# Kernel tuning notes

Hardware: AMD Instinct MI355X
Metric: run time of the kernel (lower is better)

Reference implementation:

```python
import jax, jax.numpy as jnp
import numpy as np


def _avg_conv(x, k):
    # depthwise k x k box filter, same padding (torch F.conv2d groups=C)
    C = x.shape[1]
    w = jnp.ones((C, 1, k, k), x.dtype) / (k * k)
    return jax.lax.conv_general_dilated(
        x, w, window_strides=(1, 1),
        padding=[(k // 2, k // 2), (k // 2, k // 2)],
        feature_group_count=C,
        dimension_numbers=('NCHW', 'OIHW', 'NCHW'))


def _shift_feat(where, features, neig_avg_size):
    # Faithful port of shiftFeat: edge-replicate shift + 1e-4 mask on padded strip,
    # then depthwise box average when neig_avg_size > 1. dilation is overridden to
    # neig_avg_size // 2 when neig_avg_size > 1 (as in the torch code).
    B, C, H, W = features.shape
    d = neig_avg_size // 2 if neig_avg_size > 1 else 1
    dt = features.dtype
    PAD = jnp.asarray(1e-4, dt)
    if where == 'none':
        fs = features
        m = jnp.ones((B, 1, H, W), dt)
    elif where == 'left':
        pad = jnp.broadcast_to(features[:, :, :, -1:], (B, C, H, d))
        fs = jnp.concatenate([features[:, :, :, d:], pad], axis=3)
        m = jnp.concatenate([jnp.ones((B, 1, H, W - d), dt), jnp.full((B, 1, H, d), PAD, dt)], axis=3)
    elif where == 'right':
        pad = jnp.broadcast_to(features[:, :, :, :1], (B, C, H, d))
        fs = jnp.concatenate([pad, features[:, :, :, :-d]], axis=3)
        m = jnp.concatenate([jnp.full((B, 1, H, d), PAD, dt), jnp.ones((B, 1, H, W - d), dt)], axis=3)
    elif where == 'bot':
        pad = jnp.broadcast_to(features[:, :, :1, :], (B, C, d, W))
        fs = jnp.concatenate([pad, features[:, :, :-d, :]], axis=2)
        m = jnp.concatenate([jnp.full((B, 1, d, W), PAD, dt), jnp.ones((B, 1, H - d, W), dt)], axis=2)
    elif where == 'top':
        pad = jnp.broadcast_to(features[:, :, -1:, :], (B, C, d, W))
        fs = jnp.concatenate([features[:, :, d:, :], pad], axis=2)
        m = jnp.concatenate([jnp.ones((B, 1, H - d, W), dt), jnp.full((B, 1, d, W), PAD, dt)], axis=2)
    else:
        raise ValueError('Unknown position')
    if neig_avg_size > 1:
        fs = _avg_conv(fs, neig_avg_size)
    # torch takes mask.mean(dim=1, keepdim=True); mask is constant across channels
    return fs, m


def _cos_sim(f1, m1, f2, m2):
    num = (f1 * f2 * m1 * m2).sum(axis=1, keepdims=True)
    den = (jnp.sqrt(((m1 * f1) ** 2).sum(axis=1, keepdims=True))
           * jnp.sqrt(((m2 * f2) ** 2).sum(axis=1, keepdims=True)))
    return num / den


def _total_sim(features, k):
    f1, m1 = _shift_feat('right', features, k)
    f2, m2 = _shift_feat('left', features, k)
    horiz = _cos_sim(f1, m1, f2, m2)
    f1, m1 = _shift_feat('top', features, k)
    f2, m2 = _shift_feat('bot', features, k)
    verti = _cos_sim(f1, m1, f2, m2)
    return (horiz + verti) / 2  # [B,1,H,W]


def setup_inputs() -> dict:
    key = jax.random.key(0)
    features = jax.random.normal(key, (16, 512, 56, 56), dtype=jnp.float32)
    return {"features": features, "patch_sim_neiref_neisimavgsize": 3}


def reference(features, patch_sim_neiref_neisimavgsize):
    return _total_sim(features, patch_sim_neiref_neisimavgsize)
```

## Files before the change

### kernel.cpp

```cpp
#include <hip/hip_runtime.h>
#include <hip/hip_bf16.h>

#define BB 16
#define CC 512
#define HH 56
#define WW 56
#define HW (HH * WW)
#define NPIX (BB * HW)
#define CGROUPS 8

typedef float v4f __attribute__((ext_vector_type(4)));

__device__ __forceinline__ float shfl64(float v, int srcLane) {
    return __shfl(v, srcLane, 64);
}

template <int NITER, bool WRITE_OUT>
__global__ __launch_bounds__(256, 4) void ComputeTotalSim_84267258347855_kernel(
    const float* __restrict__ feat, float* __restrict__ ws, float* __restrict__ out) {
    const int wave = threadIdx.x >> 6;
    const int lane = threadIdx.x & 63;
    const int sc = lane >> 4;
    const int q = lane & 15;
    const int qs = (q <= 13) ? q : 13;
    const int x0 = 4 * qs;
    const int b = blockIdx.z;
    const int cg = blockIdx.x;
    const int y = blockIdx.y * 4 + wave;

    const float mym = (y >= 1) ? 1.f : 0.f;
    const float myp = (y <= HH - 2) ? 1.f : 0.f;
    const float mxm0 = (q == 0) ? 0.f : 1.f;
    const float mxp3 = (q >= 13) ? 0.f : 1.f;

    const int ry0 = (y - 2 < 0) ? 0 : y - 2;
    const int ry1 = (y - 1 < 0) ? 0 : y - 1;
    const int ry3 = (y + 1 > HH - 1) ? HH - 1 : y + 1;
    const int ry4 = (y + 2 > HH - 1) ? HH - 1 : y + 2;
    const int o0 = ry0 * WW + x0, o1 = ry1 * WW + x0, o2 = y * WW + x0,
              o3 = ry3 * WW + x0, o4 = ry4 * WW + x0;

    const float* p = feat + ((size_t)b * CC + (size_t)cg * (4 * NITER) + sc) * HW;

    float sA0 = 0, sA1 = 0, sA2 = 0, sA3 = 0;
    float sB0 = 0, sB1 = 0, sB2 = 0, sB3 = 0;
    float sC0 = 0, sC1 = 0, sC2 = 0, sC3 = 0;
    float sD0 = 0, sD1 = 0, sD2 = 0, sD3 = 0;
    float sE0 = 0, sE1 = 0, sE2 = 0, sE3 = 0;
    float sF0 = 0, sF1 = 0, sF2 = 0, sF3 = 0;

#define STEP(A0, A1, A2, A3, A4)                                                \
    {                                                                           \
        const float Vx = fmaf(mym, A1.x, fmaf(myp, A3.x, A2.x));                \
        const float Vy = fmaf(mym, A1.y, fmaf(myp, A3.y, A2.y));                \
        const float Vz = fmaf(mym, A1.z, fmaf(myp, A3.z, A2.z));                \
        const float Vw = fmaf(mym, A1.w, fmaf(myp, A3.w, A2.w));                \
        const float t3x = fmaf(mym, A2.x, fmaf(myp, A4.x, A3.x));               \
        const float t3y = fmaf(mym, A2.y, fmaf(myp, A4.y, A3.y));               \
        const float t3z = fmaf(mym, A2.z, fmaf(myp, A4.z, A3.z));               \
        const float t3w = fmaf(mym, A2.w, fmaf(myp, A4.w, A3.w));               \
        const float t4x = fmaf(mym, A0.x, fmaf(myp, A2.x, A1.x));               \
        const float t4y = fmaf(mym, A0.y, fmaf(myp, A2.y, A1.y));               \
        const float t4z = fmaf(mym, A0.z, fmaf(myp, A2.z, A1.z));               \
        const float t4w = fmaf(mym, A0.w, fmaf(myp, A2.w, A1.w));               \
        float Vm2 = shfl64(Vz, lane - 1), Vm1 = shfl64(Vw, lane - 1);           \
        float Vp4 = shfl64(Vx, lane + 1), Vp5 = shfl64(Vy, lane + 1);           \
        float w3m = shfl64(t3w, lane - 1), w3p = shfl64(t3x, lane + 1);         \
        float w4m = shfl64(t4w, lane - 1), w4p = shfl64(t4x, lane + 1);         \
        if (q == 0) { Vm2 = Vx; Vm1 = Vx; w3m = t3x; w4m = t4x; }               \
        if (q >= 13) { Vp4 = Vw; Vp5 = Vw; w3p = t3w; w4p = t4w; }              \
        const float f10 = fmaf(mxm0, Vm2, Vm1 + Vx);                            \
        const float f11 = Vm1 + Vx + Vy;                                        \
        const float f12 = Vx + Vy + Vz;                                         \
        const float f13 = fmaf(mxp3, Vw, Vy + Vz);                              \
        const float f20 = fmaf(mxm0, Vx, Vy + Vz);                              \
        const float f21 = Vy + Vz + Vw;                                         \
        const float f22 = Vz + Vw + Vp4;                                        \
        const float f23 = fmaf(mxp3, Vp5, Vw + Vp4);                            \
        const float f30 = fmaf(mxm0, w3m, t3x + t3y);                           \
        const float f31 = t3x + t3y + t3z;                                      \
        const float f32 = t3y + t3z + t3w;                                      \
        const float f33 = fmaf(mxp3, w3p, t3z + t3w);                           \
        const float f40 = fmaf(mxm0, w4m, t4x + t4y);                           \
        const float f41 = t4x + t4y + t4z;                                      \
        const float f42 = t4y + t4z + t4w;                                      \
        const float f43 = fmaf(mxp3, w4p, t4z + t4w);                           \
        sA0 = fmaf(f10, f20, sA0); sA1 = fmaf(f11, f21, sA1);                   \
        sA2 = fmaf(f12, f22, sA2); sA3 = fmaf(f13, f23, sA3);                   \
        sB0 = fmaf(f10, f10, sB0); sB1 = fmaf(f11, f11, sB1);                   \
        sB2 = fmaf(f12, f12, sB2); sB3 = fmaf(f13, f13, sB3);                   \
        sC0 = fmaf(f20, f20, sC0); sC1 = fmaf(f21, f21, sC1);                   \
        sC2 = fmaf(f22, f22, sC2); sC3 = fmaf(f23, f23, sC3);                   \
        sD0 = fmaf(f30, f40, sD0); sD1 = fmaf(f31, f41, sD1);                   \
        sD2 = fmaf(f32, f42, sD2); sD3 = fmaf(f33, f43, sD3);                   \
        sE0 = fmaf(f30, f30, sE0); sE1 = fmaf(f31, f31, sE1);                   \
        sE2 = fmaf(f32, f32, sE2); sE3 = fmaf(f33, f33, sE3);                   \
        sF0 = fmaf(f40, f40, sF0); sF1 = fmaf(f41, f41, sF1);                   \
        sF2 = fmaf(f42, f42, sF2); sF3 = fmaf(f43, f43, sF3);                   \
    }

#define LOAD5(R0, R1, R2, R3, R4, PC)                                                      \
    asm volatile("global_load_dwordx4 %0, %1, off offset:-448" : "=&v"(R0) : "v"(PC));     \
    asm volatile("global_load_dwordx4 %0, %1, off offset:-224" : "=&v"(R1) : "v"(PC));     \
    asm volatile("global_load_dwordx4 %0, %1, off"             : "=&v"(R2) : "v"(PC));     \
    asm volatile("global_load_dwordx4 %0, %1, off offset:224"  : "=&v"(R3) : "v"(PC));     \
    asm volatile("global_load_dwordx4 %0, %1, off offset:448"  : "=&v"(R4) : "v"(PC));

#define WAITV(N)                                          \
    asm volatile("s_waitcnt vmcnt(" #N ")" ::: "memory"); \
    __builtin_amdgcn_sched_barrier(0);

    v4f A0, A1, A2, A3, A4, B0, B1, B2, B3, B4;

    if (blockIdx.y >= 1 && blockIdx.y <= 12) {
        const float* pc = p + o2;
        LOAD5(A0, A1, A2, A3, A4, pc); pc += 4 * HW;
        LOAD5(B0, B1, B2, B3, B4, pc); pc += 4 * HW;
        for (int k = 0; k + 4 <= NITER; k += 2) {
            WAITV(5);
            STEP(A0, A1, A2, A3, A4);
            LOAD5(A0, A1, A2, A3, A4, pc); pc += 4 * HW;
            WAITV(5);
            STEP(B0, B1, B2, B3, B4);
            LOAD5(B0, B1, B2, B3, B4, pc); pc += 4 * HW;
        }
        WAITV(5);
        STEP(A0, A1, A2, A3, A4);
        WAITV(0);
        STEP(B0, B1, B2, B3, B4);
    } else {
        A0 = *(const v4f*)(p + o0); A1 = *(const v4f*)(p + o1);
        A2 = *(const v4f*)(p + o2); A3 = *(const v4f*)(p + o3);
        A4 = *(const v4f*)(p + o4);
        p += 4 * HW;
        for (int k = 0; k + 2 <= NITER; k += 2) {
            B0 = *(const v4f*)(p + o0); B1 = *(const v4f*)(p + o1);
            B2 = *(const v4f*)(p + o2); B3 = *(const v4f*)(p + o3);
            B4 = *(const v4f*)(p + o4);
            STEP(A0, A1, A2, A3, A4);
            const float* pn = (k + 2 < NITER) ? p + 4 * HW : p;
            A0 = *(const v4f*)(pn + o0); A1 = *(const v4f*)(pn + o1);
            A2 = *(const v4f*)(pn + o2); A3 = *(const v4f*)(pn + o3);
            A4 = *(const v4f*)(pn + o4);
            STEP(B0, B1, B2, B3, B4);
            p = pn + 4 * HW;
        }
    }
#undef STEP
#undef LOAD5
#undef WAITV

#define RED2(v) { v += __shfl_xor(v, 16, 64); v += __shfl_xor(v, 32, 64); }
    RED2(sA0) RED2(sA1) RED2(sA2) RED2(sA3)
    RED2(sB0) RED2(sB1) RED2(sB2) RED2(sB3)
    RED2(sC0) RED2(sC1) RED2(sC2) RED2(sC3)
    RED2(sD0) RED2(sD1) RED2(sD2) RED2(sD3)
    RED2(sE0) RED2(sE1) RED2(sE2) RED2(sE3)
    RED2(sF0) RED2(sF1) RED2(sF2) RED2(sF3)
#undef RED2

    if (lane < 14) {
        const int pix = b * HW + y * WW + 4 * q;
        if (WRITE_OUT) {
            v4f r;
            r.x = (float)(0.5 * ((double)sA0 / sqrt((double)sB0 * (double)sC0) +
                                 (double)sD0 / sqrt((double)sE0 * (double)sF0)));
            r.y = (float)(0.5 * ((double)sA1 / sqrt((double)sB1 * (double)sC1) +
                                 (double)sD1 / sqrt((double)sE1 * (double)sF1)));
            r.z = (float)(0.5 * ((double)sA2 / sqrt((double)sB2 * (double)sC2) +
                                 (double)sD2 / sqrt((double)sE2 * (double)sF2)));
            r.w = (float)(0.5 * ((double)sA3 / sqrt((double)sB3 * (double)sC3) +
                                 (double)sD3 / sqrt((double)sE3 * (double)sF3)));
            *(v4f*)(out + pix) = r;
        } else {
            float* slab = ws + (size_t)cg * 6 * NPIX;
            *(v4f*)(slab + 0 * NPIX + pix) = (v4f){sA0, sA1, sA2, sA3};
            *(v4f*)(slab + 1 * NPIX + pix) = (v4f){sB0, sB1, sB2, sB3};
            *(v4f*)(slab + 2 * NPIX + pix) = (v4f){sC0, sC1, sC2, sC3};
            *(v4f*)(slab + 3 * NPIX + pix) = (v4f){sD0, sD1, sD2, sD3};
            *(v4f*)(slab + 4 * NPIX + pix) = (v4f){sE0, sE1, sE2, sE3};
            *(v4f*)(slab + 5 * NPIX + pix) = (v4f){sF0, sF1, sF2, sF3};
        }
    }
}

__global__ void ComputeTotalSim_finalize(const float* __restrict__ ws,
                                         float* __restrict__ out) {
    const int i = blockIdx.x * blockDim.x + threadIdx.x;
    if (i < NPIX) {
        double a0 = 0, a1 = 0, a2 = 0, a3 = 0, a4 = 0, a5 = 0;
#pragma unroll
        for (int cg = 0; cg < CGROUPS; ++cg) {
            const float* slab = ws + (size_t)cg * 6 * NPIX;
            a0 += slab[0 * NPIX + i];
            a1 += slab[1 * NPIX + i];
            a2 += slab[2 * NPIX + i];
            a3 += slab[3 * NPIX + i];
            a4 += slab[4 * NPIX + i];
            a5 += slab[5 * NPIX + i];
        }
        out[i] = (float)(0.5 * (a0 / sqrt(a1 * a2) + a3 / sqrt(a4 * a5)));
    }
}

extern "C" void kernel_launch(void* const* d_in, const int* in_sizes, int n_in,
                              void* d_out, int out_size, void* d_ws, size_t ws_size,
                              hipStream_t stream) {
    const float* feat = (const float*)d_in[0];
    float* out = (float*)d_out;

    const size_t need = (size_t)CGROUPS * 6 * NPIX * sizeof(float);
    if (ws_size >= need) {
        dim3 grid(CGROUPS, HH / 4, BB);
        ComputeTotalSim_84267258347855_kernel<CC / (4 * CGROUPS), false>
            <<<grid, 256, 0, stream>>>(feat, (float*)d_ws, out);
        ComputeTotalSim_finalize<<<(NPIX + 255) / 256, 256, 0, stream>>>(
            (const float*)d_ws, out);
    } else {
        dim3 grid(1, HH / 4, BB);
        ComputeTotalSim_84267258347855_kernel<CC / 4, true>
            <<<grid, 256, 0, stream>>>(feat, nullptr, out);
    }
}
```

Before: 34.10 us.

## Compute two output rows per wave with shared vertical sums and doubled channel groups

Each wave now produces two adjacent output rows. It loads six input rows instead of five per row and shares the vertical 3-row sums between the two rows' shifted box filters. This cuts global loads per output row from five to three and reuses intermediate sums. Channel groups go from 8 to 16 to keep the grid size up while blocks handle 8 rows. The cost is double the accumulator registers and a larger workspace and finalize reduction, which may lower occupancy.

```diff
diff --git a/kernel.cpp b/kernel.cpp
--- a/kernel.cpp
+++ b/kernel.cpp
@@ -7,7 +7,7 @@
 #define WW 56
 #define HW (HH * WW)
 #define NPIX (BB * HW)
-#define CGROUPS 8
+#define CGROUPS 16
 
 typedef float v4f __attribute__((ext_vector_type(4)));
 
@@ -20,147 +20,196 @@
     const float* __restrict__ feat, float* __restrict__ ws, float* __restrict__ out) {
     const int wave = threadIdx.x >> 6;
     const int lane = threadIdx.x & 63;
+    const int q = lane & 15;
     const int sc = lane >> 4;
-    const int q = lane & 15;
     const int qs = (q <= 13) ? q : 13;
     const int x0 = 4 * qs;
     const int b = blockIdx.z;
     const int cg = blockIdx.x;
-    const int y = blockIdx.y * 4 + wave;
-
-    const float mym = (y >= 1) ? 1.f : 0.f;
-    const float myp = (y <= HH - 2) ? 1.f : 0.f;
+    const int ys = blockIdx.y * 8 + 2 * wave;
+
     const float mxm0 = (q == 0) ? 0.f : 1.f;
     const float mxp3 = (q >= 13) ? 0.f : 1.f;
 
-    const int ry0 = (y - 2 < 0) ? 0 : y - 2;
-    const int ry1 = (y - 1 < 0) ? 0 : y - 1;
-    const int ry3 = (y + 1 > HH - 1) ? HH - 1 : y + 1;
-    const int ry4 = (y + 2 > HH - 1) ? HH - 1 : y + 2;
-    const int o0 = ry0 * WW + x0, o1 = ry1 * WW + x0, o2 = y * WW + x0,
-              o3 = ry3 * WW + x0, o4 = ry4 * WW + x0;
-
     const float* p = feat + ((size_t)b * CC + (size_t)cg * (4 * NITER) + sc) * HW;
 
-    float sA0 = 0, sA1 = 0, sA2 = 0, sA3 = 0;
-    float sB0 = 0, sB1 = 0, sB2 = 0, sB3 = 0;
-    float sC0 = 0, sC1 = 0, sC2 = 0, sC3 = 0;
-    float sD0 = 0, sD1 = 0, sD2 = 0, sD3 = 0;
-    float sE0 = 0, sE1 = 0, sE2 = 0, sE3 = 0;
-    float sF0 = 0, sF1 = 0, sF2 = 0, sF3 = 0;
-
-#define STEP(A0, A1, A2, A3, A4)                                                \
-    {                                                                           \
-        const float Vx = fmaf(mym, A1.x, fmaf(myp, A3.x, A2.x));                \
-        const float Vy = fmaf(mym, A1.y, fmaf(myp, A3.y, A2.y));                \
-        const float Vz = fmaf(mym, A1.z, fmaf(myp, A3.z, A2.z));                \
-        const float Vw = fmaf(mym, A1.w, fmaf(myp, A3.w, A2.w));                \
-        const float t3x = fmaf(mym, A2.x, fmaf(myp, A4.x, A3.x));               \
-        const float t3y = fmaf(mym, A2.y, fmaf(myp, A4.y, A3.y));               \
-        const float t3z = fmaf(mym, A2.z, fmaf(myp, A4.z, A3.z));               \
-        const float t3w = fmaf(mym, A2.w, fmaf(myp, A4.w, A3.w));               \
-        const float t4x = fmaf(mym, A0.x, fmaf(myp, A2.x, A1.x));               \
-        const float t4y = fmaf(mym, A0.y, fmaf(myp, A2.y, A1.y));               \
-        const float t4z = fmaf(mym, A0.z, fmaf(myp, A2.z, A1.z));               \
-        const float t4w = fmaf(mym, A0.w, fmaf(myp, A2.w, A1.w));               \
-        float Vm2 = shfl64(Vz, lane - 1), Vm1 = shfl64(Vw, lane - 1);           \
-        float Vp4 = shfl64(Vx, lane + 1), Vp5 = shfl64(Vy, lane + 1);           \
-        float w3m = shfl64(t3w, lane - 1), w3p = shfl64(t3x, lane + 1);         \
-        float w4m = shfl64(t4w, lane - 1), w4p = shfl64(t4x, lane + 1);         \
-        if (q == 0) { Vm2 = Vx; Vm1 = Vx; w3m = t3x; w4m = t4x; }               \
-        if (q >= 13) { Vp4 = Vw; Vp5 = Vw; w3p = t3w; w4p = t4w; }              \
-        const float f10 = fmaf(mxm0, Vm2, Vm1 + Vx);                            \
-        const float f11 = Vm1 + Vx + Vy;                                        \
-        const float f12 = Vx + Vy + Vz;                                         \
-        const float f13 = fmaf(mxp3, Vw, Vy + Vz);                              \
-        const float f20 = fmaf(mxm0, Vx, Vy + Vz);                              \
-        const float f21 = Vy + Vz + Vw;                                         \
-        const float f22 = Vz + Vw + Vp4;                                        \
-        const float f23 = fmaf(mxp3, Vp5, Vw + Vp4);                            \
-        const float f30 = fmaf(mxm0, w3m, t3x + t3y);                           \
-        const float f31 = t3x + t3y + t3z;                                      \
-        const float f32 = t3y + t3z + t3w;                                      \
-        const float f33 = fmaf(mxp3, w3p, t3z + t3w);                           \
-        const float f40 = fmaf(mxm0, w4m, t4x + t4y);                           \
-        const float f41 = t4x + t4y + t4z;                                      \
-        const float f42 = t4y + t4z + t4w;                                      \
-        const float f43 = fmaf(mxp3, w4p, t4z + t4w);                           \
-        sA0 = fmaf(f10, f20, sA0); sA1 = fmaf(f11, f21, sA1);                   \
-        sA2 = fmaf(f12, f22, sA2); sA3 = fmaf(f13, f23, sA3);                   \
-        sB0 = fmaf(f10, f10, sB0); sB1 = fmaf(f11, f11, sB1);                   \
-        sB2 = fmaf(f12, f12, sB2); sB3 = fmaf(f13, f13, sB3);                   \
-        sC0 = fmaf(f20, f20, sC0); sC1 = fmaf(f21, f21, sC1);                   \
-        sC2 = fmaf(f22, f22, sC2); sC3 = fmaf(f23, f23, sC3);                   \
-        sD0 = fmaf(f30, f40, sD0); sD1 = fmaf(f31, f41, sD1);                   \
-        sD2 = fmaf(f32, f42, sD2); sD3 = fmaf(f33, f43, sD3);                   \
-        sE0 = fmaf(f30, f30, sE0); sE1 = fmaf(f31, f31, sE1);                   \
-        sE2 = fmaf(f32, f32, sE2); sE3 = fmaf(f33, f33, sE3);                   \
-        sF0 = fmaf(f40, f40, sF0); sF1 = fmaf(f41, f41, sF1);                   \
-        sF2 = fmaf(f42, f42, sF2); sF3 = fmaf(f43, f43, sF3);                   \
-    }
-
-#define LOAD5(R0, R1, R2, R3, R4, PC)                                                      \
+    float sA0 = 0, sA1 = 0, sA2 = 0, sA3 = 0, sB0 = 0, sB1 = 0, sB2 = 0, sB3 = 0;
+    float sC0 = 0, sC1 = 0, sC2 = 0, sC3 = 0, sD0 = 0, sD1 = 0, sD2 = 0, sD3 = 0;
+    float sE0 = 0, sE1 = 0, sE2 = 0, sE3 = 0, sF0 = 0, sF1 = 0, sF2 = 0, sF3 = 0;
+    float tA0 = 0, tA1 = 0, tA2 = 0, tA3 = 0, tB0 = 0, tB1 = 0, tB2 = 0, tB3 = 0;
+    float tC0 = 0, tC1 = 0, tC2 = 0, tC3 = 0, tD0 = 0, tD1 = 0, tD2 = 0, tD3 = 0;
+    float tE0 = 0, tE1 = 0, tE2 = 0, tE3 = 0, tF0 = 0, tF1 = 0, tF2 = 0, tF3 = 0;
+
+#define SHARED2(R0, R1, R2, R3, R4, R5)                                          \
+    {                                                                            \
+        const v4f t12 = R1 + R2, t34 = R3 + R4;                                  \
+        const v4f Sa = R0 + t12, Sb = t12 + R3, Sc = t34 + R2, Sd = t34 + R5;    \
+        float aL = shfl64(Sa.w, lane - 1), aR = shfl64(Sa.x, lane + 1);          \
+        float bL2 = shfl64(Sb.z, lane - 1), bL1 = shfl64(Sb.w, lane - 1);        \
+        float bR1 = shfl64(Sb.x, lane + 1), bR2 = shfl64(Sb.y, lane + 1);        \
+        float cL2 = shfl64(Sc.z, lane - 1), cL1 = shfl64(Sc.w, lane - 1);        \
+        float cR1 = shfl64(Sc.x, lane + 1), cR2 = shfl64(Sc.y, lane + 1);        \
+        float dL = shfl64(Sd.w, lane - 1), dR = shfl64(Sd.x, lane + 1);          \
+        if (q == 0) { aL = Sa.x; bL2 = Sb.x; bL1 = Sb.x; cL2 = Sc.x; cL1 = Sc.x; dL = Sd.x; } \
+        if (q >= 13) { aR = Sa.w; bR1 = Sb.w; bR2 = Sb.w; cR1 = Sc.w; cR2 = Sc.w; dR = Sd.w; } \
+        {                                        \
+            const float f10 = fmaf(mxm0, bL2, bL1 + Sb.x), f11 = bL1 + Sb.x + Sb.y;  \
+            const float f12 = Sb.x + Sb.y + Sb.z, f13 = fmaf(mxp3, Sb.w, Sb.y + Sb.z); \
+            const float f20 = fmaf(mxm0, Sb.x, Sb.y + Sb.z), f21 = Sb.y + Sb.z + Sb.w; \
+            const float f22 = Sb.z + Sb.w + bR1, f23 = fmaf(mxp3, bR2, Sb.w + bR1);  \
+            const float f30 = fmaf(mxm0, cL1, Sc.x + Sc.y), f31 = Sc.x + Sc.y + Sc.z; \
+            const float f32 = Sc.y + Sc.z + Sc.w, f33 = fmaf(mxp3, cR1, Sc.z + Sc.w); \
+            const float f40 = fmaf(mxm0, aL, Sa.x + Sa.y), f41 = Sa.x + Sa.y + Sa.z; \
+            const float f42 = Sa.y + Sa.z + Sa.w, f43 = fmaf(mxp3, aR, Sa.z + Sa.w); \
+            sA0 = fmaf(f10, f20, sA0); sA1 = fmaf(f11, f21, sA1);                \
+            sA2 = fmaf(f12, f22, sA2); sA3 = fmaf(f13, f23, sA3);                \
+            sB0 = fmaf(f10, f10, sB0); sB1 = fmaf(f11, f11, sB1);                \
+            sB2 = fmaf(f12, f12, sB2); sB3 = fmaf(f13, f13, sB3);                \
+            sC0 = fmaf(f20, f20, sC0); sC1 = fmaf(f21, f21, sC1);                \
+            sC2 = fmaf(f22, f22, sC2); sC3 = fmaf(f23, f23, sC3);                \
+            sD0 = fmaf(f30, f40, sD0); sD1 = fmaf(f31, f41, sD1);                \
+            sD2 = fmaf(f32, f42, sD2); sD3 = fmaf(f33, f43, sD3);                \
+            sE0 = fmaf(f30, f30, sE0); sE1 = fmaf(f31, f31, sE1);                \
+            sE2 = fmaf(f32, f32, sE2); sE3 = fmaf(f33, f33, sE3);                \
+            sF0 = fmaf(f40, f40, sF0); sF1 = fmaf(f41, f41, sF1);                \
+            sF2 = fmaf(f42, f42, sF2); sF3 = fmaf(f43, f43, sF3);                \
+        }                                                                        \
+        {                                      \
+            const float f10 = fmaf(mxm0, cL2, cL1 + Sc.x), f11 = cL1 + Sc.x + Sc.y;  \
+            const float f12 = Sc.x + Sc.y + Sc.z, f13 = fmaf(mxp3, Sc.w, Sc.y + Sc.z); \
+            const float f20 = fmaf(mxm0, Sc.x, Sc.y + Sc.z), f21 = Sc.y + Sc.z + Sc.w; \
+            const float f22 = Sc.z + Sc.w + cR1, f23 = fmaf(mxp3, cR2, Sc.w + cR1);  \
+            const float f30 = fmaf(mxm0, dL, Sd.x + Sd.y), f31 = Sd.x + Sd.y + Sd.z; \
+            const float f32 = Sd.y + Sd.z + Sd.w, f33 = fmaf(mxp3, dR, Sd.z + Sd.w); \
+            const float f40 = fmaf(mxm0, bL1, Sb.x + Sb.y), f41 = Sb.x + Sb.y + Sb.z; \
+            const float f42 = Sb.y + Sb.z + Sb.w, f43 = fmaf(mxp3, bR1, Sb.z + Sb.w); \
+            tA0 = fmaf(f10, f20, tA0); tA1 = fmaf(f11, f21, tA1);                \
+            tA2 = fmaf(f12, f22, tA2); tA3 = fmaf(f13, f23, tA3);                \
+            tB0 = fmaf(f10, f10, tB0); tB1 = fmaf(f11, f11, tB1);                \
+            tB2 = fmaf(f12, f12, tB2); tB3 = fmaf(f13, f13, tB3);                \
+            tC0 = fmaf(f20, f20, tC0); tC1 = fmaf(f21, f21, tC1);                \
+            tC2 = fmaf(f22, f22, tC2); tC3 = fmaf(f23, f23, tC3);                \
+            tD0 = fmaf(f30, f40, tD0); tD1 = fmaf(f31, f41, tD1);                \
+            tD2 = fmaf(f32, f42, tD2); tD3 = fmaf(f33, f43, tD3);                \
+            tE0 = fmaf(f30, f30, tE0); tE1 = fmaf(f31, f31, tE1);                \
+            tE2 = fmaf(f32, f32, tE2); tE3 = fmaf(f33, f33, tE3);                \
+            tF0 = fmaf(f40, f40, tF0); tF1 = fmaf(f41, f41, tF1);                \
+            tF2 = fmaf(f42, f42, tF2); tF3 = fmaf(f43, f43, tF3);                \
+        }                                                                        \
+    }
+
+#define STEPB(A0_, A1_, A2_, A3_, A4_, MYM, MYP, P)                              \
+    {                                                                            \
+        const float Vx = fmaf(MYM, A1_.x, fmaf(MYP, A3_.x, A2_.x));              \
+        const float Vy = fmaf(MYM, A1_.y, fmaf(MYP, A3_.y, A2_.y));              \
+        const float Vz = fmaf(MYM, A1_.z, fmaf(MYP, A3_.z, A2_.z));              \
+        const float Vw = fmaf(MYM, A1_.w, fmaf(MYP, A3_.w, A2_.w));              \
+        const float u3x = fmaf(MYM, A2_.x, fmaf(MYP, A4_.x, A3_.x));             \
+        const float u3y = fmaf(MYM, A2_.y, fmaf(MYP, A4_.y, A3_.y));             \
+        const float u3z = fmaf(MYM, A2_.z, fmaf(MYP, A4_.z, A3_.z));             \
+        const float u3w = fmaf(MYM, A2_.w, fmaf(MYP, A4_.w, A3_.w));             \
+        const float u4x = fmaf(MYM, A0_.x, fmaf(MYP, A2_.x, A1_.x));             \
+        const float u4y = fmaf(MYM, A0_.y, fmaf(MYP, A2_.y, A1_.y));             \
+        const float u4z = fmaf(MYM, A0_.z, fmaf(MYP, A2_.z, A1_.z));             \
+        const float u4w = fmaf(MYM, A0_.w, fmaf(MYP, A2_.w, A1_.w));             \
+        float Vm2 = shfl64(Vz, lane - 1), Vm1 = shfl64(Vw, lane - 1);            \
+        float Vp4 = shfl64(Vx, lane + 1), Vp5 = shfl64(Vy, lane + 1);            \
+        float w3m = shfl64(u3w, lane - 1), w3p = shfl64(u3x, lane + 1);          \
+        float w4m = shfl64(u4w, lane - 1), w4p = shfl64(u4x, lane + 1);          \
+        if (q == 0) { Vm2 = Vx; Vm1 = Vx; w3m = u3x; w4m = u4x; }                \
+        if (q >= 13) { Vp4 = Vw; Vp5 = Vw; w3p = u3w; w4p = u4w; }               \
+        const float f10 = fmaf(mxm0, Vm2, Vm1 + Vx), f11 = Vm1 + Vx + Vy;        \
+        const float f12 = Vx + Vy + Vz, f13 = fmaf(mxp3, Vw, Vy + Vz);           \
+        const float f20 = fmaf(mxm0, Vx, Vy + Vz), f21 = Vy + Vz + Vw;           \
+        const float f22 = Vz + Vw + Vp4, f23 = fmaf(mxp3, Vp5, Vw + Vp4);        \
+        const float f30 = fmaf(mxm0, w3m, u3x + u3y), f31 = u3x + u3y + u3z;     \
+        const float f32 = u3y + u3z + u3w, f33 = fmaf(mxp3, w3p, u3z + u3w);     \
+        const float f40 = fmaf(mxm0, w4m, u4x + u4y), f41 = u4x + u4y + u4z;     \
+        const float f42 = u4y + u4z + u4w, f43 = fmaf(mxp3, w4p, u4z + u4w);     \
+        P##A0 = fmaf(f10, f20, P##A0); P##A1 = fmaf(f11, f21, P##A1);            \
+        P##A2 = fmaf(f12, f22, P##A2); P##A3 = fmaf(f13, f23, P##A3);            \
+        P##B0 = fmaf(f10, f10, P##B0); P##B1 = fmaf(f11, f11, P##B1);            \
+        P##B2 = fmaf(f12, f12, P##B2); P##B3 = fmaf(f13, f13, P##B3);            \
+        P##C0 = fmaf(f20, f20, P##C0); P##C1 = fmaf(f21, f21, P##C1);            \
+        P##C2 = fmaf(f22, f22, P##C2); P##C3 = fmaf(f23, f23, P##C3);            \
+        P##D0 = fmaf(f30, f40, P##D0); P##D1 = fmaf(f31, f41, P##D1);            \
+        P##D2 = fmaf(f32, f42, P##D2); P##D3 = fmaf(f33, f43, P##D3);            \
+        P##E0 = fmaf(f30, f30, P##E0); P##E1 = fmaf(f31, f31, P##E1);            \
+        P##E2 = fmaf(f32, f32, P##E2); P##E3 = fmaf(f33, f33, P##E3);            \
+        P##F0 = fmaf(f40, f40, P##F0); P##F1 = fmaf(f41, f41, P##F1);            \
+        P##F2 = fmaf(f42, f42, P##F2); P##F3 = fmaf(f43, f43, P##F3);            \
+    }
+
+#define LOAD6(R0, R1, R2, R3, R4, R5, PC)                                                  \
     asm volatile("global_load_dwordx4 %0, %1, off offset:-448" : "=&v"(R0) : "v"(PC));     \
     asm volatile("global_load_dwordx4 %0, %1, off offset:-224" : "=&v"(R1) : "v"(PC));     \
     asm volatile("global_load_dwordx4 %0, %1, off"             : "=&v"(R2) : "v"(PC));     \
     asm volatile("global_load_dwordx4 %0, %1, off offset:224"  : "=&v"(R3) : "v"(PC));     \
-    asm volatile("global_load_dwordx4 %0, %1, off offset:448"  : "=&v"(R4) : "v"(PC));
+    asm volatile("global_load_dwordx4 %0, %1, off offset:448"  : "=&v"(R4) : "v"(PC));     \
+    asm volatile("global_load_dwordx4 %0, %1, off offset:672"  : "=&v"(R5) : "v"(PC));
 
 #define WAITV(N)                                          \
     asm volatile("s_waitcnt vmcnt(" #N ")" ::: "memory"); \
     __builtin_amdgcn_sched_barrier(0);
 
-    v4f A0, A1, A2, A3, A4, B0, B1, B2, B3, B4;
-
-    if (blockIdx.y >= 1 && blockIdx.y <= 12) {
-        const float* pc = p + o2;
-        LOAD5(A0, A1, A2, A3, A4, pc); pc += 4 * HW;
-        LOAD5(B0, B1, B2, B3, B4, pc); pc += 4 * HW;
+    if (ys >= 2 && ys <= 52) {
+        v4f A0, A1, A2, A3, A4, A5, B0, B1, B2, B3, B4, B5;
+        const float* pc = p + (ys * WW + x0);
+        LOAD6(A0, A1, A2, A3, A4, A5, pc); pc += 4 * HW;
+        LOAD6(B0, B1, B2, B3, B4, B5, pc); pc += 4 * HW;
         for (int k = 0; k + 4 <= NITER; k += 2) {
-            WAITV(5);
-            STEP(A0, A1, A2, A3, A4);
-            LOAD5(A0, A1, A2, A3, A4, pc); pc += 4 * HW;
-            WAITV(5);
-            STEP(B0, B1, B2, B3, B4);
-            LOAD5(B0, B1, B2, B3, B4, pc); pc += 4 * HW;
-        }
-        WAITV(5);
-        STEP(A0, A1, A2, A3, A4);
+            WAITV(6);
+            SHARED2(A0, A1, A2, A3, A4, A5);
+            LOAD6(A0, A1, A2, A3, A4, A5, pc); pc += 4 * HW;
+            WAITV(6);
+            SHARED2(B0, B1, B2, B3, B4, B5);
+            LOAD6(B0, B1, B2, B3, B4, B5, pc); pc += 4 * HW;
+        }
+        WAITV(6);
+        SHARED2(A0, A1, A2, A3, A4, A5);
         WAITV(0);
-        STEP(B0, B1, B2, B3, B4);
+        SHARED2(B0, B1, B2, B3, B4, B5);
     } else {
-        A0 = *(const v4f*)(p + o0); A1 = *(const v4f*)(p + o1);
-        A2 = *(const v4f*)(p + o2); A3 = *(const v4f*)(p + o3);
-        A4 = *(const v4f*)(p + o4);
-        p += 4 * HW;
-        for (int k = 0; k + 2 <= NITER; k += 2) {
-            B0 = *(const v4f*)(p + o0); B1 = *(const v4f*)(p + o1);
-            B2 = *(const v4f*)(p + o2); B3 = *(const v4f*)(p + o3);
-            B4 = *(const v4f*)(p + o4);
-            STEP(A0, A1, A2, A3, A4);
-            const float* pn = (k + 2 < NITER) ? p + 4 * HW : p;
-            A0 = *(const v4f*)(pn + o0); A1 = *(const v4f*)(pn + o1);
-            A2 = *(const v4f*)(pn + o2); A3 = *(const v4f*)(pn + o3);
-            A4 = *(const v4f*)(pn + o4);
-            STEP(B0, B1, B2, B3, B4);
-            p = pn + 4 * HW;
-        }
-    }
-#undef STEP
-#undef LOAD5
+        const float mymA = (ys >= 1) ? 1.f : 0.f;
+        const float mypA = 1.f;
+        const float mymB = 1.f;
+        const float mypB = (ys <= 53) ? 1.f : 0.f;
+        const int a0 = ((ys - 2 < 0) ? 0 : ys - 2) * WW + x0;
+        const int a1 = ((ys - 1 < 0) ? 0 : ys - 1) * WW + x0;
+        const int a2 = ys * WW + x0;
+        const int a3 = (ys + 1) * WW + x0;
+        const int a4 = ((ys + 2 > 55) ? 55 : ys + 2) * WW + x0;
+        const int b1 = a2, b2 = a3;
+        const int b0 = a1;
+        const int b3 = ((ys + 2 > 55) ? 55 : ys + 2) * WW + x0;
+        const int b4 = ((ys + 3 > 55) ? 55 : ys + 3) * WW + x0;
+        for (int k = 0; k < NITER; ++k, p += 4 * HW) {
+            const v4f r0 = *(const v4f*)(p + a0), r1 = *(const v4f*)(p + a1),
+                      r2 = *(const v4f*)(p + a2), r3 = *(const v4f*)(p + a3),
+                      r4 = *(const v4f*)(p + a4);
+            STEPB(r0, r1, r2, r3, r4, mymA, mypA, s);
+            const v4f q0 = *(const v4f*)(p + b0), q1 = *(const v4f*)(p + b1),
+                      q2 = *(const v4f*)(p + b2), q3 = *(const v4f*)(p + b3),
+                      q4 = *(const v4f*)(p + b4);
+            STEPB(q0, q1, q2, q3, q4, mymB, mypB, t);
+        }
+    }
+#undef SHARED2
+#undef STEPB
+#undef LOAD6
 #undef WAITV
 
 #define RED2(v) { v += __shfl_xor(v, 16, 64); v += __shfl_xor(v, 32, 64); }
-    RED2(sA0) RED2(sA1) RED2(sA2) RED2(sA3)
-    RED2(sB0) RED2(sB1) RED2(sB2) RED2(sB3)
-    RED2(sC0) RED2(sC1) RED2(sC2) RED2(sC3)
-    RED2(sD0) RED2(sD1) RED2(sD2) RED2(sD3)
-    RED2(sE0) RED2(sE1) RED2(sE2) RED2(sE3)
-    RED2(sF0) RED2(sF1) RED2(sF2) RED2(sF3)
+    RED2(sA0) RED2(sA1) RED2(sA2) RED2(sA3) RED2(sB0) RED2(sB1) RED2(sB2) RED2(sB3)
+    RED2(sC0) RED2(sC1) RED2(sC2) RED2(sC3) RED2(sD0) RED2(sD1) RED2(sD2) RED2(sD3)
+    RED2(sE0) RED2(sE1) RED2(sE2) RED2(sE3) RED2(sF0) RED2(sF1) RED2(sF2) RED2(sF3)
+    RED2(tA0) RED2(tA1) RED2(tA2) RED2(tA3) RED2(tB0) RED2(tB1) RED2(tB2) RED2(tB3)
+    RED2(tC0) RED2(tC1) RED2(tC2) RED2(tC3) RED2(tD0) RED2(tD1) RED2(tD2) RED2(tD3)
+    RED2(tE0) RED2(tE1) RED2(tE2) RED2(tE3) RED2(tF0) RED2(tF1) RED2(tF2) RED2(tF3)
 #undef RED2
 
     if (lane < 14) {
-        const int pix = b * HW + y * WW + 4 * q;
+        const int pix = b * HW + ys * WW + 4 * q;
         if (WRITE_OUT) {
             v4f r;
             r.x = (float)(0.5 * ((double)sA0 / sqrt((double)sB0 * (double)sC0) +
@@ -172,6 +221,15 @@
             r.w = (float)(0.5 * ((double)sA3 / sqrt((double)sB3 * (double)sC3) +
                                  (double)sD3 / sqrt((double)sE3 * (double)sF3)));
             *(v4f*)(out + pix) = r;
+            r.x = (float)(0.5 * ((double)tA0 / sqrt((double)tB0 * (double)tC0) +
+                                 (double)tD0 / sqrt((double)tE0 * (double)tF0)));
+            r.y = (float)(0.5 * ((double)tA1 / sqrt((double)tB1 * (double)tC1) +
+                                 (double)tD1 / sqrt((double)tE1 * (double)tF1)));
+            r.z = (float)(0.5 * ((double)tA2 / sqrt((double)tB2 * (double)tC2) +
+                                 (double)tD2 / sqrt((double)tE2 * (double)tF2)));
+            r.w = (float)(0.5 * ((double)tA3 / sqrt((double)tB3 * (double)tC3) +
+                                 (double)tD3 / sqrt((double)tE3 * (double)tF3)));
+            *(v4f*)(out + pix + WW) = r;
         } else {
             float* slab = ws + (size_t)cg * 6 * NPIX;
             *(v4f*)(slab + 0 * NPIX + pix) = (v4f){sA0, sA1, sA2, sA3};
@@ -180,6 +238,12 @@
             *(v4f*)(slab + 3 * NPIX + pix) = (v4f){sD0, sD1, sD2, sD3};
             *(v4f*)(slab + 4 * NPIX + pix) = (v4f){sE0, sE1, sE2, sE3};
             *(v4f*)(slab + 5 * NPIX + pix) = (v4f){sF0, sF1, sF2, sF3};
+            *(v4f*)(slab + 0 * NPIX + pix + WW) = (v4f){tA0, tA1, tA2, tA3};
+            *(v4f*)(slab + 1 * NPIX + pix + WW) = (v4f){tB0, tB1, tB2, tB3};
+            *(v4f*)(slab + 2 * NPIX + pix + WW) = (v4f){tC0, tC1, tC2, tC3};
+            *(v4f*)(slab + 3 * NPIX + pix + WW) = (v4f){tD0, tD1, tD2, tD3};
+            *(v4f*)(slab + 4 * NPIX + pix + WW) = (v4f){tE0, tE1, tE2, tE3};
+            *(v4f*)(slab + 5 * NPIX + pix + WW) = (v4f){tF0, tF1, tF2, tF3};
         }
     }
 }
@@ -211,13 +275,13 @@
 
     const size_t need = (size_t)CGROUPS * 6 * NPIX * sizeof(float);
     if (ws_size >= need) {
-        dim3 grid(CGROUPS, HH / 4, BB);
+        dim3 grid(CGROUPS, HH / 8, BB);
         ComputeTotalSim_84267258347855_kernel<CC / (4 * CGROUPS), false>
             <<<grid, 256, 0, stream>>>(feat, (float*)d_ws, out);
         ComputeTotalSim_finalize<<<(NPIX + 255) / 256, 256, 0, stream>>>(
             (const float*)d_ws, out);
     } else {
-        dim3 grid(1, HH / 4, BB);
+        dim3 grid(1, HH / 8, BB);
         ComputeTotalSim_84267258347855_kernel<CC / 4, true>
             <<<grid, 256, 0, stream>>>(feat, nullptr, out);
     }
```

Result: slower. 35.55 us (+4.2%).
